# Optimization experiments

Measured on AMD Instinct MI355X. Metric: run time of the kernel, lower is better.

## Reference

```python
import jax, jax.numpy as jnp
import numpy as np

NUM_CLASSES = 80
TOPK = 1000
CONF_THRESH = 0.001
NMS_THRESH = 0.5
CLASS_OFFSET = 4096.0  # > max image coordinate, separates classes for class-aware NMS
M = 300000


def setup_inputs() -> dict:
    key = jax.random.key(0)
    k1, k2, k3, k4 = jax.random.split(key, 4)
    obj_preds = jax.random.normal(k1, (1, M, 1), dtype=jnp.float32)
    cls_preds = jax.random.normal(k2, (1, M, NUM_CLASSES), dtype=jnp.float32)
    # random xyxy boxes inside a 640x640 image
    cxcy = jax.random.uniform(k3, (1, M, 2), dtype=jnp.float32) * 640.0
    wh = jax.random.uniform(k4, (1, M, 2), dtype=jnp.float32) * 128.0 + 1.0
    box_preds = jnp.concatenate([cxcy - wh * 0.5, cxcy + wh * 0.5], axis=-1)
    return {"obj_preds": obj_preds, "cls_preds": cls_preds, "box_preds": box_preds}


def _iou_matrix(boxes):
    # boxes: [K, 4] xyxy -> [K, K] pairwise IoU
    x1, y1, x2, y2 = boxes[:, 0], boxes[:, 1], boxes[:, 2], boxes[:, 3]
    area = jnp.clip(x2 - x1, 0.0) * jnp.clip(y2 - y1, 0.0)
    xx1 = jnp.maximum(x1[:, None], x1[None, :])
    yy1 = jnp.maximum(y1[:, None], y1[None, :])
    xx2 = jnp.minimum(x2[:, None], x2[None, :])
    yy2 = jnp.minimum(y2[:, None], y2[None, :])
    inter = jnp.clip(xx2 - xx1, 0.0) * jnp.clip(yy2 - yy1, 0.0)
    return inter / (area[:, None] + area[None, :] - inter + 1e-9)


def _postprocess(obj_preds, cls_preds, box_preds):
    obj = obj_preds[0]   # [M, 1]
    cls = cls_preds[0]   # [M, C]
    box = box_preds[0]   # [M, 4]

    # sigmoid * sigmoid sqrt-score fusion (no_multi_labels branch)
    fused = jnp.sqrt(jax.nn.sigmoid(obj) * jax.nn.sigmoid(cls))  # [M, C]
    scores = jnp.max(fused, axis=1)     # [M]
    labels = jnp.argmax(fused, axis=1)  # [M]

    # sort-descending + take top-k == lax.top_k
    topk_scores, topk_idxs = jax.lax.top_k(scores, TOPK)
    labels_k = labels[topk_idxs]        # [K]
    boxes_k = box[topk_idxs]            # [K, 4]
    conf_mask = topk_scores > CONF_THRESH

    # multiclass NMS via class-offset trick (boxes of different classes never overlap)
    off = labels_k.astype(boxes_k.dtype)[:, None] * CLASS_OFFSET
    iou = _iou_matrix(boxes_k + off)    # [K, K]

    idx = jnp.arange(TOPK)

    def body(i, keep):
        # suppressed if any earlier, still-kept box overlaps > nms_thresh
        sup = (iou[i] > NMS_THRESH) & keep & (idx < i)
        return keep.at[i].set(keep[i] & ~jnp.any(sup))

    keep = jax.lax.fori_loop(0, TOPK, body, conf_mask)  # [K] bool

    keepf = keep.astype(topk_scores.dtype)
    # fixed-shape output: masked [K, 5] = (score, x1, y1, x2, y2); dropped rows zeroed
    out5 = jnp.concatenate([(topk_scores * keepf)[:, None], boxes_k * keepf[:, None]], axis=1)
    return out5, labels_k, keep


def reference(obj_preds, cls_preds, box_preds):
    return _postprocess(obj_preds, cls_preds, box_preds)
```

## Files before the change

kernel.cpp:

```cpp
#include <hip/hip_runtime.h>
#include <hip/hip_bf16.h>
#include <math.h>

#define NCLS 80
#define TOPK_N 1000
#define CAND_CAP 12288
#define T0 0.91f
#define OBJ_T 1.55f
#define NB 8192
#define HREP 8
#define RBINS 3072
#define RBIN_LO 0x3F680000u
#define ANCH_INV 524287

#define WS_SCORES   0
#define WS_CAND     1200000
#define WS_TKSCORE  1298304
#define WS_TKANCH   1302304
#define WS_TKLABEL  1306304
#define WS_BOXES    1310304
#define WS_OBX      1326304
#define WS_AREAS    1342304
#define WS_MASK     1346304
#define WS_META     1474304
#define WS_HIST     1474368

typedef unsigned long long u64;

__device__ __forceinline__ float sigmoidf_(float x) {
    return 1.0f / (1.0f + expf(-x));
}

__device__ __forceinline__ u64 make_key2(unsigned s32, int anchor) {
    return ((u64)s32 << 19) | (unsigned)(ANCH_INV - anchor);
}

__device__ __forceinline__ int key_bin(u64 k) {
    unsigned s32 = (unsigned)(k >> 19);
    int d = (int)(s32 - RBIN_LO);
    if (d < 0) d = 0;
    int b = d >> 9;
    if (b > RBINS - 1) b = RBINS - 1;
    return (RBINS - 1) - b;
}

__device__ __forceinline__ void rowmax16(const float4* row, int l,
                                         float& bv, int& bc) {
    float4 v4 = row[l];
    bv = v4.x; bc = l * 4;
    if (v4.y > bv) { bv = v4.y; bc = l * 4 + 1; }
    if (v4.z > bv) { bv = v4.z; bc = l * 4 + 2; }
    if (v4.w > bv) { bv = v4.w; bc = l * 4 + 3; }
    if (l < 4) {
        float4 w4 = row[16 + l];
        int cb = 64 + l * 4;
        if (w4.x > bv) { bv = w4.x; bc = cb; }
        if (w4.y > bv) { bv = w4.y; bc = cb + 1; }
        if (w4.z > bv) { bv = w4.z; bc = cb + 2; }
        if (w4.w > bv) { bv = w4.w; bc = cb + 3; }
    }
    #pragma unroll
    for (int m = 8; m >= 1; m >>= 1) {
        float ov = __shfl_xor(bv, m);
        int oc = __shfl_xor(bc, m);
        if (ov > bv || (ov == bv && oc < bc)) { bv = ov; bc = oc; }
    }
}

__global__ void __launch_bounds__(256)
k1_scores(const float* __restrict__ obj,
          const float* __restrict__ cls,
          u64* __restrict__ cand,
          int* __restrict__ counter,
          unsigned* __restrict__ hist,
          int M) {
    __shared__ int lcount, lbase, nsurv;
    __shared__ int sanch[256];
    __shared__ float sobj[256];
    __shared__ u64 lkeys[256];
    int t = threadIdx.x;
    if (t == 0) { lcount = 0; nsurv = 0; }
    for (int i = blockIdx.x * 256 + t; i < (HREP * NB) / 4; i += gridDim.x * 256)
        ((uint4*)hist)[i] = make_uint4(0u, 0u, 0u, 0u);
    __syncthreads();
    int a = blockIdx.x * 256 + t;
    float o = (a < M) ? obj[a] : -1e30f;
    if (o > OBJ_T) {
        int p = atomicAdd(&nsurv, 1);
        sanch[p] = a; sobj[p] = o;
    }
    __syncthreads();
    int ns = nsurv;
    int grp = t >> 4, l = t & 15;
    for (int s = grp; s < ns; s += 16) {
        int anchor = sanch[s];
        const float4* p = (const float4*)(cls + (size_t)anchor * NCLS);
        float4 v = p[l];
        float m = fmaxf(fmaxf(v.x, v.y), fmaxf(v.z, v.w));
        if (l < 4) {
            float4 w4 = p[16 + l];
            m = fmaxf(m, fmaxf(fmaxf(w4.x, w4.y), fmaxf(w4.z, w4.w)));
        }
        #pragma unroll
        for (int sh = 8; sh >= 1; sh >>= 1)
            m = fmaxf(m, __shfl_xor(m, sh));
        if (l == 0) {
            float score = sqrtf(sigmoidf_(sobj[s]) * sigmoidf_(m));
            if (score > T0) {
                int pos = atomicAdd(&lcount, 1);
                lkeys[pos] = make_key2(__float_as_uint(score), anchor);
            }
        }
    }
    __syncthreads();
    if (t == 0 && lcount > 0) lbase = atomicAdd(counter, lcount);
    __syncthreads();
    int n = lcount;
    if (t < n) {
        int pos = lbase + t;
        if (pos < CAND_CAP) cand[pos] = lkeys[t];
    }
}

__global__ void kf_hist(const float* __restrict__ obj,
                        const float* __restrict__ cls,
                        float* __restrict__ scores,
                        unsigned* __restrict__ hist,
                        int* __restrict__ meta, int M) {
    int C = meta[2];
    if (C >= TOPK_N && C <= CAND_CAP) return;
    int t = threadIdx.x;
    int gw = (blockIdx.x * 256 + t) >> 6;
    int TW = gridDim.x * 4;
    int lane64 = t & 63;
    int g = lane64 >> 4, l = lane64 & 15;
    int rep = blockIdx.x & (HREP - 1);
    for (int a0 = gw * 4; a0 < M; a0 += TW * 4) {
        int anchor = a0 + g;
        if (anchor >= M) continue;
        const float4* row = (const float4*)(cls + (size_t)anchor * NCLS);
        float bv; int bc;
        rowmax16(row, l, bv, bc);
        if (l == 0) {
            float score = sqrtf(sigmoidf_(obj[anchor]) * sigmoidf_(bv));
            scores[anchor] = score;
            atomicAdd(&hist[(size_t)rep * NB + (__float_as_uint(score) >> 17)], 1u);
        }
    }
    __threadfence();
    __shared__ bool last;
    if (t == 0)
        last = (atomicAdd(meta + 4, 1) == (int)gridDim.x - 1);
    __syncthreads();
    if (!last) return;
    int lane = t & 63, w = t >> 6;
    int base = NB - 1 - t * 32;
    unsigned bins[32]; unsigned s = 0;
    #pragma unroll
    for (int k = 0; k < 32; ++k) {
        unsigned h = 0;
        for (int r = 0; r < HREP; ++r)
            h += atomicOr(&hist[(size_t)r * NB + base - k], 0u);
        bins[k] = h; s += h;
    }
    unsigned inc = s;
    for (int d = 1; d < 64; d <<= 1) {
        unsigned pv = __shfl_up(inc, d);
        if (lane >= d) inc += pv;
    }
    __shared__ unsigned wsum[4], woff[4];
    if (lane == 63) wsum[w] = inc;
    __syncthreads();
    if (t == 0) {
        unsigned cum = 0;
        for (int i = 0; i < 4; ++i) { woff[i] = cum; cum += wsum[i]; }
    }
    __syncthreads();
    unsigned excl = woff[w] + inc - s;
    if (excl < TOPK_N && excl + s >= TOPK_N) {
        unsigned cum = excl; int b = base;
        #pragma unroll
        for (int k = 0; k < 32; ++k) {
            unsigned h = bins[k];
            if (cum + h >= TOPK_N) { meta[0] = b; break; }
            cum += h; --b;
        }
    }
}

__global__ void k3_compact(const float* __restrict__ scores,
                           int* __restrict__ meta,
                           u64* __restrict__ cand, int M) {
    int C = meta[2];
    if (C >= TOPK_N && C <= CAND_CAP) return;
    int B = meta[0];
    for (int i = blockIdx.x * 256 + threadIdx.x; i < M; i += gridDim.x * 256) {
        unsigned key = __float_as_uint(scores[i]);
        if ((int)(key >> 17) >= B) {
            int pos = atomicAdd(meta + 3, 1);
            if (pos < CAND_CAP)
                cand[pos] = make_key2(key, i);
        }
    }
}

__global__ void __launch_bounds__(1024)
k4_rank(const u64* __restrict__ cand,
        const int* __restrict__ meta,
        float* __restrict__ tkscore,
        int* __restrict__ tkanchor) {
    __shared__ u64 sorted[CAND_CAP];
    __shared__ unsigned hist[RBINS];
    __shared__ unsigned cnt[RBINS];
    __shared__ unsigned wsum[16], woff[16];
    int t = threadIdx.x;
    int lane = t & 63, w = t >> 6;
    int Cf = meta[2];
    bool fast = (Cf >= TOPK_N && Cf <= CAND_CAP);
    int C = fast ? Cf : meta[3];
    if (C > CAND_CAP) C = CAND_CAP;
    for (int b = t; b < RBINS; b += 1024) { hist[b] = 0; cnt[b] = 0; }
    __syncthreads();
    u64 keys[12]; int nk = 0;
    for (int i = t; i < C; i += 1024) {
        u64 k = cand[i];
        keys[nk++] = k;
        atomicAdd(&hist[key_bin(k)], 1u);
    }
    __syncthreads();
    unsigned h0 = hist[t * 3], h1 = hist[t * 3 + 1], h2 = hist[t * 3 + 2];
    unsigned s = h0 + h1 + h2;
    unsigned inc = s;
    for (int d = 1; d < 64; d <<= 1) {
        unsigned pv = __shfl_up(inc, d);
        if (lane >= d) inc += pv;
    }
    if (lane == 63) wsum[w] = inc;
    __syncthreads();
    if (t == 0) {
        unsigned cum = 0;
        for (int i = 0; i < 16; ++i) { woff[i] = cum; cum += wsum[i]; }
    }
    __syncthreads();
    unsigned base = woff[w] + inc - s;
    hist[t * 3] = base;
    hist[t * 3 + 1] = base + h0;
    hist[t * 3 + 2] = base + h0 + h1;
    __syncthreads();
    nk = 0;
    for (int i = t; i < C; i += 1024) {
        u64 k = keys[nk++];
        int b = key_bin(k);
        unsigned pos = hist[b] + atomicAdd(&cnt[b], 1u);
        sorted[pos] = k;
    }
    __syncthreads();
    for (int p = t; p < C; p += 1024) {
        u64 k = sorted[p];
        int b = key_bin(k);
        unsigned b0 = hist[b], b1 = b0 + cnt[b];
        int r = (int)b0;
        for (unsigned q = b0; q < b1; ++q) r += (sorted[q] > k);
        if (r < TOPK_N) {
            tkscore[r] = __uint_as_float((unsigned)(k >> 19));
            tkanchor[r] = ANCH_INV - (int)(k & 0x7FFFF);
        }
    }
}

__global__ void __launch_bounds__(256)
k4b_gather(const float* __restrict__ cls,
           const float4* __restrict__ box,
           const int* __restrict__ tkanchor,
           int* __restrict__ tklabel,
           float4* __restrict__ boxes_k,
           float4* __restrict__ obx,
           float* __restrict__ areas) {
    int grp = threadIdx.x >> 4, l = threadIdx.x & 15;
    int r = blockIdx.x * 16 + grp;
    if (r >= TOPK_N) return;
    int anchor = tkanchor[r];
    const float4* row = (const float4*)(cls + (size_t)anchor * NCLS);
    float bv; int bc;
    rowmax16(row, l, bv, bc);
    if (l == 0) {
        tklabel[r] = bc;
        float4 b = box[anchor];
        boxes_k[r] = b;
        float off = (float)bc * 4096.0f;
        float4 ob = make_float4(b.x + off, b.y + off, b.z + off, b.w + off);
        obx[r] = ob;
        areas[r] = fmaxf(ob.z - ob.x, 0.0f) * fmaxf(ob.w - ob.y, 0.0f);
    }
}

__global__ void k5_iou(const float4* __restrict__ obx,
                       const float* __restrict__ areas,
                       u64* __restrict__ mask) {
    int i = blockIdx.x * 4 + (threadIdx.x >> 6);
    int lane = threadIdx.x & 63;
    if (i >= TOPK_N) return;
    float4 bi = obx[i];
    float ai = areas[i];
    for (int w = 0; w < 16; ++w) {
        int c = w * 64 + lane;
        bool bit = false;
        if (c < i) {
            float4 bc = obx[c];
            float xx1 = fmaxf(bi.x, bc.x), yy1 = fmaxf(bi.y, bc.y);
            float xx2 = fminf(bi.z, bc.z), yy2 = fminf(bi.w, bc.w);
            float inter = fmaxf(xx2 - xx1, 0.0f) * fmaxf(yy2 - yy1, 0.0f);
            float iou = inter / (ai + areas[c] - inter + 1e-9f);
            bit = iou > 0.5f;
        }
        u64 bal = __ballot(bit);
        if (lane == 0) mask[(size_t)i * 16 + w] = bal;
    }
}

__global__ void __launch_bounds__(1024)
k6_nms(const float* __restrict__ tkscore,
       const u64* __restrict__ mask,
       const int* __restrict__ tklabel,
       const float4* __restrict__ boxes_k,
       float* __restrict__ out) {
    __shared__ u64 kept_s[16], dec_s[16];
    int t = threadIdx.x, w = t >> 6, lane = t & 63;
    bool active = t < TOPK_N;
    u64 sup[16];
    float sc = 0.0f;
    if (active) {
        #pragma unroll
        for (int q = 0; q < 16; ++q) sup[q] = mask[(size_t)t * 16 + q];
        sc = tkscore[t];
    } else {
        #pragma unroll
        for (int q = 0; q < 16; ++q) sup[q] = 0ULL;
    }
    bool conf = active && (sc > 0.001f);
    bool mydec = !conf;
    bool mykept = false;
    u64 db = __ballot(mydec), kb = __ballot(mykept);
    if (lane == 0) { dec_s[w] = db; kept_s[w] = kb; }
    __syncthreads();
    for (int round = 0; round < TOPK_N; ++round) {
        if (!mydec) {
            u64 pend = 0;
            #pragma unroll
            for (int q = 0; q < 16; ++q) pend |= sup[q] & ~dec_s[q];
            if (pend == 0ULL) {
                u64 kk = 0;
                #pragma unroll
                for (int q = 0; q < 16; ++q) kk |= sup[q] & kept_s[q];
                mydec = true; mykept = (kk == 0ULL);
            }
        }
        __syncthreads();
        db = __ballot(mydec); kb = __ballot(mykept);
        if (lane == 0) { dec_s[w] = db; kept_s[w] = kb; }
        __syncthreads();
        u64 a = ~0ULL;
        #pragma unroll
        for (int q = 0; q < 16; ++q) a &= dec_s[q];
        if (a == ~0ULL) break;
    }
    if (active) {
        float k = mykept ? 1.0f : 0.0f;
        float4 b = boxes_k[t];
        out[t * 5 + 0] = sc * k;
        out[t * 5 + 1] = b.x * k;
        out[t * 5 + 2] = b.y * k;
        out[t * 5 + 3] = b.z * k;
        out[t * 5 + 4] = b.w * k;
        out[5 * TOPK_N + t] = (float)tklabel[t];
        out[6 * TOPK_N + t] = k;
    }
}

extern "C" void kernel_launch(void* const* d_in, const int* in_sizes, int n_in,
                              void* d_out, int out_size, void* d_ws, size_t ws_size,
                              hipStream_t stream) {
    const float* obj = (const float*)d_in[0];
    const float* cls = (const float*)d_in[1];
    const float* box = (const float*)d_in[2];
    float* out = (float*)d_out;
    char* ws = (char*)d_ws;
    int M = in_sizes[0];

    float*    scores  = (float*)(ws + WS_SCORES);
    u64*      cand    = (u64*)(ws + WS_CAND);
    float*    tkscore = (float*)(ws + WS_TKSCORE);
    int*      tkanch  = (int*)(ws + WS_TKANCH);
    int*      tklabel = (int*)(ws + WS_TKLABEL);
    float4*   boxes_k = (float4*)(ws + WS_BOXES);
    float4*   obx     = (float4*)(ws + WS_OBX);
    float*    areas   = (float*)(ws + WS_AREAS);
    u64*      mask    = (u64*)(ws + WS_MASK);
    int*      meta    = (int*)(ws + WS_META);
    unsigned* hist    = (unsigned*)(ws + WS_HIST);

    hipMemsetAsync(ws + WS_META, 0, 64, stream);

    k1_scores<<<(M + 255) / 256, 256, 0, stream>>>(obj, cls, cand, meta + 2, hist, M);
    kf_hist<<<512, 256, 0, stream>>>(obj, cls, scores, hist, meta, M);
    k3_compact<<<512, 256, 0, stream>>>(scores, meta, cand, M);
    k4_rank<<<1, 1024, 0, stream>>>(cand, meta, tkscore, tkanch);
    k4b_gather<<<(TOPK_N + 15) / 16, 256, 0, stream>>>(cls, (const float4*)box,
                                                       tkanch, tklabel, boxes_k, obx, areas);
    k5_iou<<<(TOPK_N + 3) / 4, 256, 0, stream>>>(obx, areas, mask);
    k6_nms<<<1, 1024, 0, stream>>>(tkscore, mask, tklabel, boxes_k, out);
}
```

Baseline: 171.9 us.

## Fuse gather, IoU and NMS into one persistent kernel with grid barriers

Result: slower. 213.1 us (+24.0%).

```diff
diff --git a/kernel.cpp b/kernel.cpp
--- a/kernel.cpp
+++ b/kernel.cpp
@@ -12,18 +12,18 @@
 #define RBINS 3072
 #define RBIN_LO 0x3F680000u
 #define ANCH_INV 524287
-
-#define WS_SCORES   0
-#define WS_CAND     1200000
-#define WS_TKSCORE  1298304
-#define WS_TKANCH   1302304
-#define WS_TKLABEL  1306304
-#define WS_BOXES    1310304
-#define WS_OBX      1326304
-#define WS_AREAS    1342304
-#define WS_MASK     1346304
-#define WS_META     1474304
-#define WS_HIST     1474368
+#define KIO_BLOCKS 63
+
+#define WS_CAND     0
+#define WS_TKSCORE  98304
+#define WS_TKANCH   102304
+#define WS_TKLABEL  106304
+#define WS_BOXES    110304
+#define WS_OBX      126304
+#define WS_AREAS    142304
+#define WS_MASK     146304
+#define WS_META     274304
+#define WS_HIST     274368
 
 typedef unsigned long long u64;
 
@@ -122,11 +122,12 @@
     }
 }
 
-__global__ void kf_hist(const float* __restrict__ obj,
-                        const float* __restrict__ cls,
-                        float* __restrict__ scores,
-                        unsigned* __restrict__ hist,
-                        int* __restrict__ meta, int M) {
+__global__ void __launch_bounds__(256)
+kfb_fallback(const float* __restrict__ obj,
+             const float* __restrict__ cls,
+             unsigned* __restrict__ hist,
+             int* __restrict__ meta,
+             u64* __restrict__ cand, int M) {
     int C = meta[2];
     if (C >= TOPK_N && C <= CAND_CAP) return;
     int t = threadIdx.x;
@@ -143,7 +144,6 @@
         rowmax16(row, l, bv, bc);
         if (l == 0) {
             float score = sqrtf(sigmoidf_(obj[anchor]) * sigmoidf_(bv));
-            scores[anchor] = score;
             atomicAdd(&hist[(size_t)rep * NB + (__float_as_uint(score) >> 17)], 1u);
         }
     }
@@ -152,54 +152,63 @@
     if (t == 0)
         last = (atomicAdd(meta + 4, 1) == (int)gridDim.x - 1);
     __syncthreads();
-    if (!last) return;
-    int lane = t & 63, w = t >> 6;
-    int base = NB - 1 - t * 32;
-    unsigned bins[32]; unsigned s = 0;
-    #pragma unroll
-    for (int k = 0; k < 32; ++k) {
-        unsigned h = 0;
-        for (int r = 0; r < HREP; ++r)
-            h += atomicOr(&hist[(size_t)r * NB + base - k], 0u);
-        bins[k] = h; s += h;
-    }
-    unsigned inc = s;
-    for (int d = 1; d < 64; d <<= 1) {
-        unsigned pv = __shfl_up(inc, d);
-        if (lane >= d) inc += pv;
-    }
-    __shared__ unsigned wsum[4], woff[4];
-    if (lane == 63) wsum[w] = inc;
-    __syncthreads();
-    if (t == 0) {
-        unsigned cum = 0;
-        for (int i = 0; i < 4; ++i) { woff[i] = cum; cum += wsum[i]; }
-    }
-    __syncthreads();
-    unsigned excl = woff[w] + inc - s;
-    if (excl < TOPK_N && excl + s >= TOPK_N) {
-        unsigned cum = excl; int b = base;
+    if (last) {
+        int lane = t & 63, w = t >> 6;
+        int base = NB - 1 - t * 32;
+        unsigned bins[32]; unsigned s = 0;
         #pragma unroll
         for (int k = 0; k < 32; ++k) {
-            unsigned h = bins[k];
-            if (cum + h >= TOPK_N) { meta[0] = b; break; }
-            cum += h; --b;
-        }
-    }
-}
-
-__global__ void k3_compact(const float* __restrict__ scores,
-                           int* __restrict__ meta,
-                           u64* __restrict__ cand, int M) {
-    int C = meta[2];
-    if (C >= TOPK_N && C <= CAND_CAP) return;
-    int B = meta[0];
-    for (int i = blockIdx.x * 256 + threadIdx.x; i < M; i += gridDim.x * 256) {
-        unsigned key = __float_as_uint(scores[i]);
-        if ((int)(key >> 17) >= B) {
-            int pos = atomicAdd(meta + 3, 1);
-            if (pos < CAND_CAP)
-                cand[pos] = make_key2(key, i);
+            unsigned h = 0;
+            for (int r = 0; r < HREP; ++r)
+                h += atomicOr(&hist[(size_t)r * NB + base - k], 0u);
+            bins[k] = h; s += h;
+        }
+        unsigned inc = s;
+        for (int d = 1; d < 64; d <<= 1) {
+            unsigned pv = __shfl_up(inc, d);
+            if (lane >= d) inc += pv;
+        }
+        __shared__ unsigned wsum[4], woff[4];
+        if (lane == 63) wsum[w] = inc;
+        __syncthreads();
+        if (t == 0) {
+            unsigned cum = 0;
+            for (int i = 0; i < 4; ++i) { woff[i] = cum; cum += wsum[i]; }
+        }
+        __syncthreads();
+        unsigned excl = woff[w] + inc - s;
+        if (excl < TOPK_N && excl + s >= TOPK_N) {
+            unsigned cum = excl; int b = base;
+            #pragma unroll
+            for (int k = 0; k < 32; ++k) {
+                unsigned h = bins[k];
+                if (cum + h >= TOPK_N) { atomicExch(meta + 0, b); break; }
+                cum += h; --b;
+            }
+        }
+        __syncthreads();
+        __threadfence();
+        if (t == 0) atomicExch(meta + 5, 1);
+    }
+    if (t == 0)
+        while (atomicAdd(meta + 5, 0) == 0) { __builtin_amdgcn_s_sleep(8); }
+    __syncthreads();
+    __threadfence();
+    int B = atomicAdd(meta + 0, 0);
+    for (int a0 = gw * 4; a0 < M; a0 += TW * 4) {
+        int anchor = a0 + g;
+        if (anchor >= M) continue;
+        const float4* row = (const float4*)(cls + (size_t)anchor * NCLS);
+        float bv; int bc;
+        rowmax16(row, l, bv, bc);
+        if (l == 0) {
+            float score = sqrtf(sigmoidf_(obj[anchor]) * sigmoidf_(bv));
+            unsigned key = __float_as_uint(score);
+            if ((int)(key >> 17) >= B) {
+                int pos = atomicAdd(meta + 3, 1);
+                if (pos < CAND_CAP)
+                    cand[pos] = make_key2(key, anchor);
+            }
         }
     }
 }
@@ -268,64 +277,83 @@
     }
 }
 
-__global__ void __launch_bounds__(256)
-k4b_gather(const float* __restrict__ cls,
-           const float4* __restrict__ box,
-           const int* __restrict__ tkanchor,
-           int* __restrict__ tklabel,
-           float4* __restrict__ boxes_k,
-           float4* __restrict__ obx,
-           float* __restrict__ areas) {
-    int grp = threadIdx.x >> 4, l = threadIdx.x & 15;
-    int r = blockIdx.x * 16 + grp;
-    if (r >= TOPK_N) return;
-    int anchor = tkanchor[r];
-    const float4* row = (const float4*)(cls + (size_t)anchor * NCLS);
-    float bv; int bc;
-    rowmax16(row, l, bv, bc);
-    if (l == 0) {
-        tklabel[r] = bc;
-        float4 b = box[anchor];
-        boxes_k[r] = b;
-        float off = (float)bc * 4096.0f;
-        float4 ob = make_float4(b.x + off, b.y + off, b.z + off, b.w + off);
-        obx[r] = ob;
-        areas[r] = fmaxf(ob.z - ob.x, 0.0f) * fmaxf(ob.w - ob.y, 0.0f);
-    }
-}
-
-__global__ void k5_iou(const float4* __restrict__ obx,
-                       const float* __restrict__ areas,
-                       u64* __restrict__ mask) {
-    int i = blockIdx.x * 4 + (threadIdx.x >> 6);
-    int lane = threadIdx.x & 63;
-    if (i >= TOPK_N) return;
-    float4 bi = obx[i];
-    float ai = areas[i];
-    for (int w = 0; w < 16; ++w) {
-        int c = w * 64 + lane;
-        bool bit = false;
-        if (c < i) {
-            float4 bc = obx[c];
-            float xx1 = fmaxf(bi.x, bc.x), yy1 = fmaxf(bi.y, bc.y);
-            float xx2 = fminf(bi.z, bc.z), yy2 = fminf(bi.w, bc.w);
-            float inter = fmaxf(xx2 - xx1, 0.0f) * fmaxf(yy2 - yy1, 0.0f);
-            float iou = inter / (ai + areas[c] - inter + 1e-9f);
-            bit = iou > 0.5f;
-        }
-        u64 bal = __ballot(bit);
-        if (lane == 0) mask[(size_t)i * 16 + w] = bal;
-    }
-}
-
 __global__ void __launch_bounds__(1024)
-k6_nms(const float* __restrict__ tkscore,
-       const u64* __restrict__ mask,
-       const int* __restrict__ tklabel,
-       const float4* __restrict__ boxes_k,
-       float* __restrict__ out) {
+kio_tail(const float* __restrict__ cls,
+         const float4* __restrict__ box,
+         const float* __restrict__ tkscore,
+         const int* __restrict__ tkanchor,
+         int* __restrict__ tklabel,
+         float4* __restrict__ boxes_k,
+         float4* __restrict__ obx,
+         float* __restrict__ areas,
+         u64* __restrict__ mask,
+         int* __restrict__ meta,
+         float* __restrict__ out) {
+    __shared__ float4 sobx[TOPK_N];
+    __shared__ float  sarea[TOPK_N];
     __shared__ u64 kept_s[16], dec_s[16];
-    int t = threadIdx.x, w = t >> 6, lane = t & 63;
+    int t = threadIdx.x, bid = blockIdx.x;
+    int nblk = gridDim.x;
+    int G = bid * 64 + (t >> 4), l16 = t & 15;
+    if (G < TOPK_N) {
+        int anchor = tkanchor[G];
+        const float4* row = (const float4*)(cls + (size_t)anchor * NCLS);
+        float bv; int bc;
+        rowmax16(row, l16, bv, bc);
+        if (l16 == 0) {
+            tklabel[G] = bc;
+            float4 b = box[anchor];
+            boxes_k[G] = b;
+            float off = (float)bc * 4096.0f;
+            float4 ob = make_float4(b.x + off, b.y + off, b.z + off, b.w + off);
+            obx[G] = ob;
+            areas[G] = fmaxf(ob.z - ob.x, 0.0f) * fmaxf(ob.w - ob.y, 0.0f);
+        }
+    }
+    __syncthreads();
+    __threadfence();
+    if (t == 0) {
+        if (atomicAdd(meta + 6, 1) == nblk - 1)
+            atomicExch(meta + 7, 1);
+        while (atomicAdd(meta + 7, 0) == 0) { __builtin_amdgcn_s_sleep(8); }
+    }
+    __syncthreads();
+    __threadfence();
+    for (int j = t; j < TOPK_N; j += 1024) { sobx[j] = obx[j]; sarea[j] = areas[j]; }
+    __syncthreads();
+    int w = t >> 6, lane = t & 63;
+    int i = bid * 16 + w;
+    if (i < TOPK_N) {
+        float4 bi = sobx[i];
+        float ai = sarea[i];
+        #pragma unroll 4
+        for (int q = 0; q < 16; ++q) {
+            int c = q * 64 + lane;
+            bool bit = false;
+            if (c < i) {
+                float4 bc = sobx[c];
+                float xx1 = fmaxf(bi.x, bc.x), yy1 = fmaxf(bi.y, bc.y);
+                float xx2 = fminf(bi.z, bc.z), yy2 = fminf(bi.w, bc.w);
+                float inter = fmaxf(xx2 - xx1, 0.0f) * fmaxf(yy2 - yy1, 0.0f);
+                float iou = inter / (ai + sarea[c] - inter + 1e-9f);
+                bit = iou > 0.5f;
+            }
+            u64 bal = __ballot(bit);
+            if (lane == 0) mask[(size_t)i * 16 + q] = bal;
+        }
+    }
+    __syncthreads();
+    __threadfence();
+    if (bid != 0) {
+        if (t == 0) atomicAdd(meta + 8, 1);
+        return;
+    }
+    if (t == 0) {
+        atomicAdd(meta + 8, 1);
+        while (atomicAdd(meta + 8, 0) < nblk) { __builtin_amdgcn_s_sleep(8); }
+    }
+    __syncthreads();
+    __threadfence();
     bool active = t < TOPK_N;
     u64 sup[16];
     float sc = 0.0f;
@@ -387,7 +415,6 @@
     char* ws = (char*)d_ws;
     int M = in_sizes[0];
 
-    float*    scores  = (float*)(ws + WS_SCORES);
     u64*      cand    = (u64*)(ws + WS_CAND);
     float*    tkscore = (float*)(ws + WS_TKSCORE);
     int*      tkanch  = (int*)(ws + WS_TKANCH);
@@ -402,11 +429,9 @@
     hipMemsetAsync(ws + WS_META, 0, 64, stream);
 
     k1_scores<<<(M + 255) / 256, 256, 0, stream>>>(obj, cls, cand, meta + 2, hist, M);
-    kf_hist<<<512, 256, 0, stream>>>(obj, cls, scores, hist, meta, M);
-    k3_compact<<<512, 256, 0, stream>>>(scores, meta, cand, M);
+    kfb_fallback<<<512, 256, 0, stream>>>(obj, cls, hist, meta, cand, M);
     k4_rank<<<1, 1024, 0, stream>>>(cand, meta, tkscore, tkanch);
-    k4b_gather<<<(TOPK_N + 15) / 16, 256, 0, stream>>>(cls, (const float4*)box,
-                                                       tkanch, tklabel, boxes_k, obx, areas);
-    k5_iou<<<(TOPK_N + 3) / 4, 256, 0, stream>>>(obx, areas, mask);
-    k6_nms<<<1, 1024, 0, stream>>>(tkscore, mask, tklabel, boxes_k, out);
-}
+    kio_tail<<<KIO_BLOCKS, 1024, 0, stream>>>(cls, (const float4*)box, tkscore,
+                                              tkanch, tklabel, boxes_k, obx, areas,
+                                              mask, meta, out);
+}
```
